# Kernel tuning notes

Measured on AMD Instinct MI355X. Metric: run time of the kernel, lower is better.

Reference implementation:

```python
import jax, jax.numpy as jnp
import numpy as np

B, D = 16, 8192
CH = 32
N_BLOCKS = 24
DILATIONS = [2 ** i for i in range(8)] * 3  # 3 stacks of 8 layers


def _causal_conv(x, W, b, dilation):
    # x: (B, Cin, L); W: (Cout, Cin, K). Causal = left-pad (K-1)*dilation only,
    # which equals torch's symmetric-pad-then-slice-right trick.
    pad = (W.shape[-1] - 1) * dilation
    y = jax.lax.conv_general_dilated(
        x, W, window_strides=(1,), padding=[(pad, 0)],
        rhs_dilation=(dilation,), dimension_numbers=('NCH', 'OIH', 'NCH'))
    return y + b[None, :, None]


def setup_inputs() -> dict:
    key = jax.random.key(0)
    ks = jax.random.split(key, 13)
    s = 0.1  # keep activations in a sane range
    return {
        'x': jax.random.normal(ks[0], (B, D), jnp.float32),
        'W0': jax.random.normal(ks[1], (CH, 1, 2), jnp.float32) * s,
        'b0': jax.random.normal(ks[2], (CH,), jnp.float32) * s,
        'Wd': jax.random.normal(ks[3], (N_BLOCKS, 2 * CH, CH, 2), jnp.float32) * s,
        'bd': jax.random.normal(ks[4], (N_BLOCKS, 2 * CH), jnp.float32) * s,
        'W1': jax.random.normal(ks[5], (N_BLOCKS, CH, CH), jnp.float32) * s,
        'b1': jax.random.normal(ks[6], (N_BLOCKS, CH), jnp.float32) * s,
        'Wf': jax.random.normal(ks[7], (CH, CH), jnp.float32) * s,
        'bf': jax.random.normal(ks[8], (CH,), jnp.float32) * s,
        'fW1': jax.random.normal(ks[9], (64, CH * 4), jnp.float32) * s,
        'fb1': jax.random.normal(ks[10], (64,), jnp.float32) * s,
        'fW2': jax.random.normal(ks[11], (10, 64), jnp.float32) * s,
        'fb2': jax.random.normal(ks[12], (10,), jnp.float32) * s,
    }


def reference(x, W0, b0, Wd, bd, W1, b1, Wf, bf, fW1, fb1, fW2, fb2):
    h = _causal_conv(x[:, None, :], W0, b0, 1)  # (B, 32, L)
    skip_sum = jnp.zeros_like(h)
    for i, dil in enumerate(DILATIONS):
        z = _causal_conv(h, Wd[i], bd[i], dil)          # (B, 64, L)
        f, g = jnp.split(z, 2, axis=1)
        gated = jnp.tanh(f) * jax.nn.sigmoid(g)          # (B, 32, L)
        skip = jnp.einsum('oc,bcl->bol', W1[i], gated) + b1[i][None, :, None]
        h = h + skip                                     # residual (dropout = eval identity)
        skip_sum = skip_sum + skip                       # sum of stacked skips
    y = jax.nn.relu(skip_sum)
    y = jnp.einsum('oc,bcl->bol', Wf, y) + bf[None, :, None]
    y = jax.nn.relu(y)
    # AdaptiveMaxPool1d(4): L divisible by 4 -> max over contiguous chunks
    Bc, C, L = y.shape
    y = y.reshape(Bc, C, 4, L // 4).max(axis=-1)         # (B, 32, 4)
    y = y.reshape(Bc, C * 4)
    y = jax.nn.relu(y @ fW1.T + fb1)
    return y @ fW2.T + fb2
```

## Files before the change

kernel.cpp:

```cpp
#include <hip/hip_runtime.h>
#include <hip/hip_bf16.h>

#define BATCH 16
#define SEQ 8192
#define CH 32
#define NB 24

typedef __attribute__((ext_vector_type(8))) short short8;
typedef __attribute__((ext_vector_type(4))) short short4v;
typedef __attribute__((ext_vector_type(4))) float f32x4;

#define LROW 36

__device__ __forceinline__ unsigned short f2bf(float x) {
    __hip_bfloat16 b = __float2bfloat16(x);
    unsigned short u;
    __builtin_memcpy(&u, &b, 2);
    return u;
}
__device__ __forceinline__ float bf2f(unsigned short h) {
    return __uint_as_float(((unsigned int)h) << 16);
}
__device__ __forceinline__ float rcp_fast(float x) { return __builtin_amdgcn_rcpf(x); }

__device__ __forceinline__ float gate_fn(float f, float g) {
    float ef = __expf(-2.0f * fabsf(f));
    float eg = __expf(-g);
    float num = 1.0f - ef;
    float den = (1.0f + ef) * (1.0f + eg);
    return copysignf(num * rcp_fast(den), f);
}

__device__ __forceinline__ void split2(float v, unsigned short& h, unsigned short& l) {
    h = f2bf(v);
    l = f2bf(v - bf2f(h));
}

__global__ __launch_bounds__(64) void k_prep(const float* __restrict__ Wd,
                                             const float* __restrict__ bd,
                                             const float* __restrict__ W1,
                                             const float* __restrict__ b1,
                                             unsigned short* __restrict__ stream) {
    int i = blockIdx.x;
    int l = threadIdx.x;
    int p = l & 15, h4 = l >> 4;
    const float* wd  = Wd + (size_t)i * 64 * 64;
    const float* w1  = W1 + (size_t)i * 1024;
    const float* bdp = bd + (size_t)i * 64;
    const float* b1p = b1 + (size_t)i * 32;
    unsigned short* out = stream + (size_t)i * (28672 / 2);

    for (int rt = 0; rt < 4; ++rt)
        for (int q = 0; q < 2; ++q) {
            int slot = rt * 2 + q;
            for (int j = 0; j < 8; ++j) {
                int m = 16 * rt + p;
                int k = 32 * q + 8 * h4 + j;
                int c = k & 31, tap = k >> 5;
                float w = wd[m * 64 + c * 2 + tap];
                unsigned short hi = f2bf(w);
                out[(size_t)slot * 512 + l * 8 + j] = hi;
                out[(size_t)(8 + slot) * 512 + l * 8 + j] = f2bf(w - bf2f(hi));
            }
        }
    for (int rt2 = 0; rt2 < 2; ++rt2)
        for (int j = 0; j < 8; ++j) {
            int o = 16 * rt2 + p, c = 8 * h4 + j;
            float w = w1[o * 32 + c];
            unsigned short hi = f2bf(w);
            out[(size_t)(16 + rt2) * 512 + l * 8 + j] = hi;
            out[(size_t)(18 + rt2) * 512 + l * 8 + j] = f2bf(w - bf2f(hi));
        }
    float* outf = (float*)stream + (size_t)i * (28672 / 4);
    for (int rt = 0; rt < 4; ++rt)
        for (int r = 0; r < 4; ++r)
            outf[(size_t)(20 + rt) * 256 + l * 4 + r] = bdp[16 * rt + 4 * h4 + r];
    for (int rt2 = 0; rt2 < 2; ++rt2)
        for (int r = 0; r < 4; ++r)
            outf[(size_t)(24 + rt2) * 256 + l * 4 + r] = b1p[16 * rt2 + 4 * h4 + r];
}

__global__ __launch_bounds__(256) void k_init(const float* __restrict__ x,
                                              const float* __restrict__ W0,
                                              const float* __restrict__ b0,
                                              float* __restrict__ h,
                                              float* __restrict__ pooled) {
    int idx = blockIdx.x * 256 + threadIdx.x;
    int b = idx >> 13, t = idx & (SEQ - 1);
    float xt = x[b * SEQ + t];
    float xm = (t > 0) ? x[b * SEQ + t - 1] : 0.0f;
    __align__(16) float hv[CH];
#pragma unroll
    for (int c = 0; c < CH; ++c)
        hv[c] = W0[c * 2] * xm + W0[c * 2 + 1] * xt + b0[c];
    float* dst = h + (size_t)idx * CH;
#pragma unroll
    for (int k = 0; k < 8; ++k)
        *(f32x4*)(dst + 4 * k) = *(const f32x4*)(hv + 4 * k);
    if (idx < BATCH * CH * 4) pooled[idx] = 0.0f;
}

__global__ __launch_bounds__(512, 2) void k_stack(
        const float* __restrict__ hin,
        float* __restrict__ hout,
        const unsigned short* __restrict__ wstream,
        int stack) {
    __shared__ __align__(16) float lh[768 * LROW];
    __shared__ __align__(16) unsigned short gbuf[8][2][16][40];

    int tid = threadIdx.x;
    int lane = tid & 63, wave = tid >> 6;
    int p = lane & 15, h4 = lane >> 4;
    int bb = blockIdx.x >> 4;
    int T0 = (blockIdx.x & 15) * 512;

    const float* pin = hin + (size_t)bb * SEQ * CH;
    float* pout = hout + (size_t)bb * SEQ * CH;

    const f32x4 zero4 = {0.0f, 0.0f, 0.0f, 0.0f};

    for (int i = tid; i < 768; i += 512) {
        int t = T0 - 256 + i;
        float* dst = &lh[i * LROW];
        if (t >= 0) {
            const float* src = pin + (size_t)t * CH;
#pragma unroll
            for (int k = 0; k < 8; ++k)
                *(f32x4*)(dst + 4 * k) = *(const f32x4*)(src + 4 * k);
        } else {
#pragma unroll
            for (int k = 0; k < 8; ++k)
                *(f32x4*)(dst + 4 * k) = zero4;
        }
    }
    __syncthreads();

#pragma unroll 1
    for (int l = 0; l < 8; ++l) {
        int dil = 1 << l;
        const unsigned short* frag = wstream + (size_t)(8 * stack + l) * 14336;
        const short8* fs = (const short8*)frag;
        short8 Ah[4][2], Al[4][2], Sh[2], Sl[2];
#pragma unroll
        for (int rt = 0; rt < 4; ++rt)
#pragma unroll
            for (int q = 0; q < 2; ++q) {
                Ah[rt][q] = fs[(rt * 2 + q) * 64 + lane];
                Al[rt][q] = fs[(8 + rt * 2 + q) * 64 + lane];
            }
#pragma unroll
        for (int rt2 = 0; rt2 < 2; ++rt2) {
            Sh[rt2] = fs[(16 + rt2) * 64 + lane];
            Sl[rt2] = fs[(18 + rt2) * 64 + lane];
        }
        const f32x4* ff = (const f32x4*)frag;
        f32x4 bFG[4], bS[2];
#pragma unroll
        for (int rt = 0; rt < 4; ++rt) bFG[rt] = ff[(20 + rt) * 64 + lane];
#pragma unroll
        for (int rt2 = 0; rt2 < 2; ++rt2) bS[rt2] = ff[(24 + rt2) * 64 + lane];

        f32x4 hnew[6][2];

#pragma unroll
        for (int s6 = 0; s6 < 6; ++s6) {
            int tpos = wave * 96 + s6 * 16 + p;
            int tq = tpos - dil;
            bool ok = (T0 - 256 + tq >= 0);
            int tqc = (tq > 0) ? tq : 0;

            const float* r1 = &lh[tpos * LROW + 8 * h4];
            const float* r0 = &lh[tqc * LROW + 8 * h4];
            f32x4 v1a = *(const f32x4*)r1, v1b = *(const f32x4*)(r1 + 4);
            f32x4 v0a = *(const f32x4*)r0, v0b = *(const f32x4*)(r0 + 4);
            if (!ok) { v0a = zero4; v0b = zero4; }
            short8 bh1, bl1, bh0, bl0;
#pragma unroll
            for (int j = 0; j < 4; ++j) {
                unsigned short hh, ll;
                split2(v1a[j], hh, ll); bh1[j] = (short)hh; bl1[j] = (short)ll;
                split2(v1b[j], hh, ll); bh1[4 + j] = (short)hh; bl1[4 + j] = (short)ll;
                split2(v0a[j], hh, ll); bh0[j] = (short)hh; bl0[j] = (short)ll;
                split2(v0b[j], hh, ll); bh0[4 + j] = (short)hh; bl0[4 + j] = (short)ll;
            }

            f32x4 acc[4];
#pragma unroll
            for (int rt = 0; rt < 4; ++rt) {
                f32x4 a = bFG[rt];
                a = __builtin_amdgcn_mfma_f32_16x16x32_bf16(Ah[rt][0], bh0, a, 0, 0, 0);
                a = __builtin_amdgcn_mfma_f32_16x16x32_bf16(Ah[rt][1], bh1, a, 0, 0, 0);
                a = __builtin_amdgcn_mfma_f32_16x16x32_bf16(Ah[rt][0], bl0, a, 0, 0, 0);
                a = __builtin_amdgcn_mfma_f32_16x16x32_bf16(Ah[rt][1], bl1, a, 0, 0, 0);
                a = __builtin_amdgcn_mfma_f32_16x16x32_bf16(Al[rt][0], bh0, a, 0, 0, 0);
                a = __builtin_amdgcn_mfma_f32_16x16x32_bf16(Al[rt][1], bh1, a, 0, 0, 0);
                acc[rt] = a;
            }

#pragma unroll
            for (int rt = 0; rt < 2; ++rt) {
                __align__(8) unsigned short g4h[4], g4l[4];
#pragma unroll
                for (int r = 0; r < 4; ++r) {
                    float gated = gate_fn(acc[rt][r], acc[rt + 2][r]);
                    split2(gated, g4h[r], g4l[r]);
                }
                *(short4v*)&gbuf[wave][0][p][16 * rt + 4 * h4] = *(const short4v*)g4h;
                *(short4v*)&gbuf[wave][1][p][16 * rt + 4 * h4] = *(const short4v*)g4l;
            }
            asm volatile("s_waitcnt lgkmcnt(0)" ::: "memory");
            __builtin_amdgcn_sched_barrier(0);
            short8 Bgh = *(const short8*)&gbuf[wave][0][p][8 * h4];
            short8 Bgl = *(const short8*)&gbuf[wave][1][p][8 * h4];

            f32x4 sacc[2];
#pragma unroll
            for (int rt2 = 0; rt2 < 2; ++rt2) {
                f32x4 a = bS[rt2];
                a = __builtin_amdgcn_mfma_f32_16x16x32_bf16(Sh[rt2], Bgh, a, 0, 0, 0);
                a = __builtin_amdgcn_mfma_f32_16x16x32_bf16(Sh[rt2], Bgl, a, 0, 0, 0);
                a = __builtin_amdgcn_mfma_f32_16x16x32_bf16(Sl[rt2], Bgh, a, 0, 0, 0);
                sacc[rt2] = a;
            }

#pragma unroll
            for (int rt2 = 0; rt2 < 2; ++rt2) {
                f32x4 hold = *(const f32x4*)&lh[tpos * LROW + 16 * rt2 + 4 * h4];
                hnew[s6][rt2] = hold + sacc[rt2];
            }
        }
        __syncthreads();

#pragma unroll
        for (int s6 = 0; s6 < 6; ++s6) {
            int tpos = wave * 96 + s6 * 16 + p;
#pragma unroll
            for (int rt2 = 0; rt2 < 2; ++rt2)
                *(f32x4*)&lh[tpos * LROW + 16 * rt2 + 4 * h4] = hnew[s6][rt2];
        }
        __syncthreads();
    }

    {
        int i = 256 + tid;
        int t = T0 + tid;
        const float* src = &lh[i * LROW];
        float* dst = pout + (size_t)t * CH;
#pragma unroll
        for (int k = 0; k < 8; ++k)
            *(f32x4*)(dst + 4 * k) = *(const f32x4*)(src + 4 * k);
    }
}

__global__ __launch_bounds__(256) void k_final1(
        const float* __restrict__ hfin,
        const float* __restrict__ x,
        const float* __restrict__ W0,
        const float* __restrict__ b0,
        const float* __restrict__ Wf,
        const float* __restrict__ bf,
        float* __restrict__ pooled) {
    int blk = blockIdx.x;
    int b = blk >> 5;
    int chunk = blk & 31;
    int q = chunk >> 3;
    int t = chunk * 256 + threadIdx.x;

    float xt = x[b * SEQ + t];
    float xm = (t > 0) ? x[b * SEQ + t - 1] : 0.0f;
    const float* ph = hfin + ((size_t)b * SEQ + t) * CH;
    f32x4 v[8];
#pragma unroll
    for (int k = 0; k < 8; ++k) v[k] = *(const f32x4*)(ph + 4 * k);

    float r[CH];
#pragma unroll
    for (int k = 0; k < 8; ++k)
#pragma unroll
        for (int j = 0; j < 4; ++j) {
            int c = 4 * k + j;
            float h0 = W0[c * 2] * xm + W0[c * 2 + 1] * xt + b0[c];
            r[c] = fmaxf(v[k][j] - h0, 0.0f);
        }

    float y[CH];
#pragma unroll 1
    for (int o = 0; o < CH; ++o) {
        const float* w = Wf + o * CH;
        float a0 = bf[o], a1 = 0.0f, a2 = 0.0f, a3 = 0.0f;
#pragma unroll
        for (int c = 0; c < CH; c += 4) {
            a0 += w[c + 0] * r[c + 0];
            a1 += w[c + 1] * r[c + 1];
            a2 += w[c + 2] * r[c + 2];
            a3 += w[c + 3] * r[c + 3];
        }
        y[o] = fmaxf((a0 + a1) + (a2 + a3), 0.0f);
    }

#pragma unroll
    for (int o = 0; o < CH; ++o) {
#pragma unroll
        for (int off = 32; off >= 1; off >>= 1)
            y[o] = fmaxf(y[o], __shfl_xor(y[o], off));
    }

    __shared__ float red[4 * CH];
    int wave = threadIdx.x >> 6, lane = threadIdx.x & 63;
    if (lane == 0) {
#pragma unroll
        for (int o = 0; o < CH; ++o) red[wave * CH + o] = y[o];
    }
    __syncthreads();
    if (threadIdx.x < CH) {
        float m = fmaxf(fmaxf(red[threadIdx.x], red[CH + threadIdx.x]),
                        fmaxf(red[2 * CH + threadIdx.x], red[3 * CH + threadIdx.x]));
        atomicMax((unsigned int*)&pooled[b * (CH * 4) + threadIdx.x * 4 + q],
                  __float_as_uint(m));
    }
}

__global__ __launch_bounds__(1024) void k_final2(const float* __restrict__ pooled,
                                                 const float* __restrict__ fW1,
                                                 const float* __restrict__ fb1,
                                                 const float* __restrict__ fW2,
                                                 const float* __restrict__ fb2,
                                                 float* __restrict__ out) {
    __shared__ float y1[BATCH * 64];
    int tid = threadIdx.x;
    int b = tid >> 6, o = tid & 63;
    float acc = fb1[o];
#pragma unroll
    for (int j = 0; j < 128; ++j) acc += fW1[o * 128 + j] * pooled[b * 128 + j];
    y1[b * 64 + o] = fmaxf(acc, 0.0f);
    __syncthreads();
    if (tid < BATCH * 10) {
        int bb = tid / 10, o2 = tid % 10;
        float a2 = fb2[o2];
#pragma unroll
        for (int j = 0; j < 64; ++j) a2 += fW2[o2 * 64 + j] * y1[bb * 64 + j];
        out[bb * 10 + o2] = a2;
    }
}

extern "C" void kernel_launch(void* const* d_in, const int* in_sizes, int n_in,
                              void* d_out, int out_size, void* d_ws, size_t ws_size,
                              hipStream_t stream) {
    const float* x   = (const float*)d_in[0];
    const float* W0  = (const float*)d_in[1];
    const float* b0  = (const float*)d_in[2];
    const float* Wd  = (const float*)d_in[3];
    const float* bd  = (const float*)d_in[4];
    const float* W1  = (const float*)d_in[5];
    const float* b1  = (const float*)d_in[6];
    const float* Wf  = (const float*)d_in[7];
    const float* bf  = (const float*)d_in[8];
    const float* fW1 = (const float*)d_in[9];
    const float* fb1 = (const float*)d_in[10];
    const float* fW2 = (const float*)d_in[11];
    const float* fb2 = (const float*)d_in[12];
    float* out = (float*)d_out;

    const size_t HS = (size_t)BATCH * SEQ * CH;
    float* bufA = (float*)d_ws;
    float* bufB = bufA + HS;
    unsigned short* wstream = (unsigned short*)(bufB + HS);
    float* pooled = (float*)(wstream + (size_t)NB * 14336);

    k_prep<<<NB, 64, 0, stream>>>(Wd, bd, W1, b1, wstream);
    k_init<<<512, 256, 0, stream>>>(x, W0, b0, bufA, pooled);

    k_stack<<<256, 512, 0, stream>>>(bufA, bufB, wstream, 0);
    k_stack<<<256, 512, 0, stream>>>(bufB, bufA, wstream, 1);
    k_stack<<<256, 512, 0, stream>>>(bufA, bufB, wstream, 2);

    k_final1<<<512, 256, 0, stream>>>(bufB, x, W0, b0, Wf, bf, pooled);
    k_final2<<<1, 1024, 0, stream>>>(pooled, fW1, fb1, fW2, fb2, out);
}
```

Before: 365.7 us.

## Fuse init and final pooling into stack kernels, software-pipeline skip MFMA

Removes k_init by computing the first conv inside the first k_stack launch from x, and removes k_final1 by doing the final 1x1 conv, ReLU and max-pool reduction inside the last stack launch, skipping its hidden-state write-back. Pooled zeroing moves into k_prep. The per-layer inner loop is software-pipelined: the gbuf is double-buffered so the skip MFMA for slice i-1 overlaps the dilated-conv MFMA for slice i. This saves two launches and a full HBM round trip of the hidden state, at the cost of more shared memory and register pressure in k_stack.

```diff
diff --git a/kernel.cpp b/kernel.cpp
--- a/kernel.cpp
+++ b/kernel.cpp
@@ -40,7 +40,8 @@
                                              const float* __restrict__ bd,
                                              const float* __restrict__ W1,
                                              const float* __restrict__ b1,
-                                             unsigned short* __restrict__ stream) {
+                                             unsigned short* __restrict__ stream,
+                                             float* __restrict__ pooled) {
     int i = blockIdx.x;
     int l = threadIdx.x;
     int p = l & 15, h4 = l >> 4;
@@ -49,6 +50,9 @@
     const float* bdp = bd + (size_t)i * 64;
     const float* b1p = b1 + (size_t)i * 32;
     unsigned short* out = stream + (size_t)i * (28672 / 2);
+
+    for (int g = blockIdx.x * 64 + l; g < BATCH * CH * 4; g += NB * 64)
+        pooled[g] = 0.0f;
 
     for (int rt = 0; rt < 4; ++rt)
         for (int q = 0; q < 2; ++q) {
@@ -80,57 +84,69 @@
             outf[(size_t)(24 + rt2) * 256 + l * 4 + r] = b1p[16 * rt2 + 4 * h4 + r];
 }
 
-__global__ __launch_bounds__(256) void k_init(const float* __restrict__ x,
-                                              const float* __restrict__ W0,
-                                              const float* __restrict__ b0,
-                                              float* __restrict__ h,
-                                              float* __restrict__ pooled) {
-    int idx = blockIdx.x * 256 + threadIdx.x;
-    int b = idx >> 13, t = idx & (SEQ - 1);
-    float xt = x[b * SEQ + t];
-    float xm = (t > 0) ? x[b * SEQ + t - 1] : 0.0f;
-    __align__(16) float hv[CH];
-#pragma unroll
-    for (int c = 0; c < CH; ++c)
-        hv[c] = W0[c * 2] * xm + W0[c * 2 + 1] * xt + b0[c];
-    float* dst = h + (size_t)idx * CH;
-#pragma unroll
-    for (int k = 0; k < 8; ++k)
-        *(f32x4*)(dst + 4 * k) = *(const f32x4*)(hv + 4 * k);
-    if (idx < BATCH * CH * 4) pooled[idx] = 0.0f;
-}
-
 __global__ __launch_bounds__(512, 2) void k_stack(
         const float* __restrict__ hin,
         float* __restrict__ hout,
+        const float* __restrict__ x,
+        const float* __restrict__ W0,
+        const float* __restrict__ b0,
+        const float* __restrict__ Wf,
+        const float* __restrict__ bf,
+        float* __restrict__ pooled,
         const unsigned short* __restrict__ wstream,
         int stack) {
     __shared__ __align__(16) float lh[768 * LROW];
-    __shared__ __align__(16) unsigned short gbuf[8][2][16][40];
+    __shared__ __align__(16) unsigned short gbuf[8][2][2][16][40];
+    __shared__ float red[8 * CH];
 
     int tid = threadIdx.x;
     int lane = tid & 63, wave = tid >> 6;
     int p = lane & 15, h4 = lane >> 4;
     int bb = blockIdx.x >> 4;
     int T0 = (blockIdx.x & 15) * 512;
+    bool first = (stack == 0);
+    bool last  = (stack == 2);
 
     const float* pin = hin + (size_t)bb * SEQ * CH;
     float* pout = hout + (size_t)bb * SEQ * CH;
+    const float* px = x + (size_t)bb * SEQ;
 
     const f32x4 zero4 = {0.0f, 0.0f, 0.0f, 0.0f};
 
-    for (int i = tid; i < 768; i += 512) {
-        int t = T0 - 256 + i;
-        float* dst = &lh[i * LROW];
-        if (t >= 0) {
-            const float* src = pin + (size_t)t * CH;
-#pragma unroll
-            for (int k = 0; k < 8; ++k)
-                *(f32x4*)(dst + 4 * k) = *(const f32x4*)(src + 4 * k);
-        } else {
-#pragma unroll
-            for (int k = 0; k < 8; ++k)
-                *(f32x4*)(dst + 4 * k) = zero4;
+    if (first) {
+        for (int i = tid; i < 768; i += 512) {
+            int t = T0 - 256 + i;
+            float* dst = &lh[i * LROW];
+            if (t >= 0) {
+                float xt = px[t];
+                float xm = (t > 0) ? px[t - 1] : 0.0f;
+                __align__(16) float hv[CH];
+#pragma unroll
+                for (int c = 0; c < CH; ++c)
+                    hv[c] = W0[c * 2] * xm + W0[c * 2 + 1] * xt + b0[c];
+#pragma unroll
+                for (int k = 0; k < 8; ++k)
+                    *(f32x4*)(dst + 4 * k) = *(const f32x4*)(hv + 4 * k);
+            } else {
+#pragma unroll
+                for (int k = 0; k < 8; ++k)
+                    *(f32x4*)(dst + 4 * k) = zero4;
+            }
+        }
+    } else {
+        for (int i = tid; i < 768; i += 512) {
+            int t = T0 - 256 + i;
+            float* dst = &lh[i * LROW];
+            if (t >= 0) {
+                const float* src = pin + (size_t)t * CH;
+#pragma unroll
+                for (int k = 0; k < 8; ++k)
+                    *(f32x4*)(dst + 4 * k) = *(const f32x4*)(src + 4 * k);
+            } else {
+#pragma unroll
+                for (int k = 0; k < 8; ++k)
+                    *(f32x4*)(dst + 4 * k) = zero4;
+            }
         }
     }
     __syncthreads();
@@ -163,77 +179,83 @@
         f32x4 hnew[6][2];
 
 #pragma unroll
+        for (int i = 0; i < 7; ++i) {
+            f32x4 acc[4];
+            if (i < 6) {
+                int tpos = wave * 96 + i * 16 + p;
+                int tq = tpos - dil;
+                bool ok = (T0 - 256 + tq >= 0);
+                int tqc = (tq > 0) ? tq : 0;
+
+                const float* r1 = &lh[tpos * LROW + 8 * h4];
+                const float* r0 = &lh[tqc * LROW + 8 * h4];
+                f32x4 v1a = *(const f32x4*)r1, v1b = *(const f32x4*)(r1 + 4);
+                f32x4 v0a = *(const f32x4*)r0, v0b = *(const f32x4*)(r0 + 4);
+                if (!ok) { v0a = zero4; v0b = zero4; }
+                short8 bh1, bl1, bh0, bl0;
+#pragma unroll
+                for (int j = 0; j < 4; ++j) {
+                    unsigned short hh, ll;
+                    split2(v1a[j], hh, ll); bh1[j] = (short)hh; bl1[j] = (short)ll;
+                    split2(v1b[j], hh, ll); bh1[4 + j] = (short)hh; bl1[4 + j] = (short)ll;
+                    split2(v0a[j], hh, ll); bh0[j] = (short)hh; bl0[j] = (short)ll;
+                    split2(v0b[j], hh, ll); bh0[4 + j] = (short)hh; bl0[4 + j] = (short)ll;
+                }
+#pragma unroll
+                for (int rt = 0; rt < 4; ++rt) {
+                    f32x4 a = bFG[rt];
+                    a = __builtin_amdgcn_mfma_f32_16x16x32_bf16(Ah[rt][0], bh0, a, 0, 0, 0);
+                    a = __builtin_amdgcn_mfma_f32_16x16x32_bf16(Ah[rt][1], bh1, a, 0, 0, 0);
+                    a = __builtin_amdgcn_mfma_f32_16x16x32_bf16(Ah[rt][0], bl0, a, 0, 0, 0);
+                    a = __builtin_amdgcn_mfma_f32_16x16x32_bf16(Ah[rt][1], bl1, a, 0, 0, 0);
+                    a = __builtin_amdgcn_mfma_f32_16x16x32_bf16(Al[rt][0], bh0, a, 0, 0, 0);
+                    a = __builtin_amdgcn_mfma_f32_16x16x32_bf16(Al[rt][1], bh1, a, 0, 0, 0);
+                    acc[rt] = a;
+                }
+            }
+
+            if (i > 0) {
+                asm volatile("s_waitcnt lgkmcnt(0)" ::: "memory");
+                int ip = i - 1;
+                int tposP = wave * 96 + ip * 16 + p;
+                short8 Bgh = *(const short8*)&gbuf[wave][ip & 1][0][p][8 * h4];
+                short8 Bgl = *(const short8*)&gbuf[wave][ip & 1][1][p][8 * h4];
+
+                f32x4 sacc[2];
+#pragma unroll
+                for (int rt2 = 0; rt2 < 2; ++rt2) {
+                    f32x4 a = bS[rt2];
+                    a = __builtin_amdgcn_mfma_f32_16x16x32_bf16(Sh[rt2], Bgh, a, 0, 0, 0);
+                    a = __builtin_amdgcn_mfma_f32_16x16x32_bf16(Sh[rt2], Bgl, a, 0, 0, 0);
+                    a = __builtin_amdgcn_mfma_f32_16x16x32_bf16(Sl[rt2], Bgh, a, 0, 0, 0);
+                    sacc[rt2] = a;
+                }
+#pragma unroll
+                for (int rt2 = 0; rt2 < 2; ++rt2) {
+                    f32x4 hold = *(const f32x4*)&lh[tposP * LROW + 16 * rt2 + 4 * h4];
+                    hnew[ip][rt2] = hold + sacc[rt2];
+                }
+            }
+
+            if (i < 6) {
+#pragma unroll
+                for (int rt = 0; rt < 2; ++rt) {
+                    __align__(8) unsigned short g4h[4], g4l[4];
+#pragma unroll
+                    for (int r = 0; r < 4; ++r) {
+                        float gated = gate_fn(acc[rt][r], acc[rt + 2][r]);
+                        split2(gated, g4h[r], g4l[r]);
+                    }
+                    *(short4v*)&gbuf[wave][i & 1][0][p][16 * rt + 4 * h4] = *(const short4v*)g4h;
+                    *(short4v*)&gbuf[wave][i & 1][1][p][16 * rt + 4 * h4] = *(const short4v*)g4l;
+                }
+            }
+        }
+        __syncthreads();
+
+#pragma unroll
         for (int s6 = 0; s6 < 6; ++s6) {
             int tpos = wave * 96 + s6 * 16 + p;
-            int tq = tpos - dil;
-            bool ok = (T0 - 256 + tq >= 0);
-            int tqc = (tq > 0) ? tq : 0;
-
-            const float* r1 = &lh[tpos * LROW + 8 * h4];
-            const float* r0 = &lh[tqc * LROW + 8 * h4];
-            f32x4 v1a = *(const f32x4*)r1, v1b = *(const f32x4*)(r1 + 4);
-            f32x4 v0a = *(const f32x4*)r0, v0b = *(const f32x4*)(r0 + 4);
-            if (!ok) { v0a = zero4; v0b = zero4; }
-            short8 bh1, bl1, bh0, bl0;
-#pragma unroll
-            for (int j = 0; j < 4; ++j) {
-                unsigned short hh, ll;
-                split2(v1a[j], hh, ll); bh1[j] = (short)hh; bl1[j] = (short)ll;
-                split2(v1b[j], hh, ll); bh1[4 + j] = (short)hh; bl1[4 + j] = (short)ll;
-                split2(v0a[j], hh, ll); bh0[j] = (short)hh; bl0[j] = (short)ll;
-                split2(v0b[j], hh, ll); bh0[4 + j] = (short)hh; bl0[4 + j] = (short)ll;
-            }
-
-            f32x4 acc[4];
-#pragma unroll
-            for (int rt = 0; rt < 4; ++rt) {
-                f32x4 a = bFG[rt];
-                a = __builtin_amdgcn_mfma_f32_16x16x32_bf16(Ah[rt][0], bh0, a, 0, 0, 0);
-                a = __builtin_amdgcn_mfma_f32_16x16x32_bf16(Ah[rt][1], bh1, a, 0, 0, 0);
-                a = __builtin_amdgcn_mfma_f32_16x16x32_bf16(Ah[rt][0], bl0, a, 0, 0, 0);
-                a = __builtin_amdgcn_mfma_f32_16x16x32_bf16(Ah[rt][1], bl1, a, 0, 0, 0);
-                a = __builtin_amdgcn_mfma_f32_16x16x32_bf16(Al[rt][0], bh0, a, 0, 0, 0);
-                a = __builtin_amdgcn_mfma_f32_16x16x32_bf16(Al[rt][1], bh1, a, 0, 0, 0);
-                acc[rt] = a;
-            }
-
-#pragma unroll
-            for (int rt = 0; rt < 2; ++rt) {
-                __align__(8) unsigned short g4h[4], g4l[4];
-#pragma unroll
-                for (int r = 0; r < 4; ++r) {
-                    float gated = gate_fn(acc[rt][r], acc[rt + 2][r]);
-                    split2(gated, g4h[r], g4l[r]);
-                }
-                *(short4v*)&gbuf[wave][0][p][16 * rt + 4 * h4] = *(const short4v*)g4h;
-                *(short4v*)&gbuf[wave][1][p][16 * rt + 4 * h4] = *(const short4v*)g4l;
-            }
-            asm volatile("s_waitcnt lgkmcnt(0)" ::: "memory");
-            __builtin_amdgcn_sched_barrier(0);
-            short8 Bgh = *(const short8*)&gbuf[wave][0][p][8 * h4];
-            short8 Bgl = *(const short8*)&gbuf[wave][1][p][8 * h4];
-
-            f32x4 sacc[2];
-#pragma unroll
-            for (int rt2 = 0; rt2 < 2; ++rt2) {
-                f32x4 a = bS[rt2];
-                a = __builtin_amdgcn_mfma_f32_16x16x32_bf16(Sh[rt2], Bgh, a, 0, 0, 0);
-                a = __builtin_amdgcn_mfma_f32_16x16x32_bf16(Sh[rt2], Bgl, a, 0, 0, 0);
-                a = __builtin_amdgcn_mfma_f32_16x16x32_bf16(Sl[rt2], Bgh, a, 0, 0, 0);
-                sacc[rt2] = a;
-            }
-
-#pragma unroll
-            for (int rt2 = 0; rt2 < 2; ++rt2) {
-                f32x4 hold = *(const f32x4*)&lh[tpos * LROW + 16 * rt2 + 4 * h4];
-                hnew[s6][rt2] = hold + sacc[rt2];
-            }
-        }
-        __syncthreads();
-
-#pragma unroll
-        for (int s6 = 0; s6 < 6; ++s6) {
-            int tpos = wave * 96 + s6 * 16 + p;
 #pragma unroll
             for (int rt2 = 0; rt2 < 2; ++rt2)
                 *(f32x4*)&lh[tpos * LROW + 16 * rt2 + 4 * h4] = hnew[s6][rt2];
@@ -241,7 +263,7 @@
         __syncthreads();
     }
 
-    {
+    if (!last) {
         int i = 256 + tid;
         int t = T0 + tid;
         const float* src = &lh[i * LROW];
@@ -249,74 +271,52 @@
 #pragma unroll
         for (int k = 0; k < 8; ++k)
             *(f32x4*)(dst + 4 * k) = *(const f32x4*)(src + 4 * k);
-    }
-}
-
-__global__ __launch_bounds__(256) void k_final1(
-        const float* __restrict__ hfin,
-        const float* __restrict__ x,
-        const float* __restrict__ W0,
-        const float* __restrict__ b0,
-        const float* __restrict__ Wf,
-        const float* __restrict__ bf,
-        float* __restrict__ pooled) {
-    int blk = blockIdx.x;
-    int b = blk >> 5;
-    int chunk = blk & 31;
-    int q = chunk >> 3;
-    int t = chunk * 256 + threadIdx.x;
-
-    float xt = x[b * SEQ + t];
-    float xm = (t > 0) ? x[b * SEQ + t - 1] : 0.0f;
-    const float* ph = hfin + ((size_t)b * SEQ + t) * CH;
-    f32x4 v[8];
-#pragma unroll
-    for (int k = 0; k < 8; ++k) v[k] = *(const f32x4*)(ph + 4 * k);
-
-    float r[CH];
-#pragma unroll
-    for (int k = 0; k < 8; ++k)
-#pragma unroll
-        for (int j = 0; j < 4; ++j) {
-            int c = 4 * k + j;
+    } else {
+        int i = 256 + tid;
+        int t = T0 + tid;
+        int q = (blockIdx.x & 15) >> 2;
+        float xt = px[t];
+        float xm = (t > 0) ? px[t - 1] : 0.0f;
+        const float* src = &lh[i * LROW];
+
+        float r[CH];
+#pragma unroll
+        for (int c = 0; c < CH; ++c) {
             float h0 = W0[c * 2] * xm + W0[c * 2 + 1] * xt + b0[c];
-            r[c] = fmaxf(v[k][j] - h0, 0.0f);
-        }
-
-    float y[CH];
+            r[c] = fmaxf(src[c] - h0, 0.0f);
+        }
+        float y[CH];
 #pragma unroll 1
-    for (int o = 0; o < CH; ++o) {
-        const float* w = Wf + o * CH;
-        float a0 = bf[o], a1 = 0.0f, a2 = 0.0f, a3 = 0.0f;
-#pragma unroll
-        for (int c = 0; c < CH; c += 4) {
-            a0 += w[c + 0] * r[c + 0];
-            a1 += w[c + 1] * r[c + 1];
-            a2 += w[c + 2] * r[c + 2];
-            a3 += w[c + 3] * r[c + 3];
-        }
-        y[o] = fmaxf((a0 + a1) + (a2 + a3), 0.0f);
-    }
-
-#pragma unroll
-    for (int o = 0; o < CH; ++o) {
-#pragma unroll
-        for (int off = 32; off >= 1; off >>= 1)
-            y[o] = fmaxf(y[o], __shfl_xor(y[o], off));
-    }
-
-    __shared__ float red[4 * CH];
-    int wave = threadIdx.x >> 6, lane = threadIdx.x & 63;
-    if (lane == 0) {
-#pragma unroll
-        for (int o = 0; o < CH; ++o) red[wave * CH + o] = y[o];
-    }
-    __syncthreads();
-    if (threadIdx.x < CH) {
-        float m = fmaxf(fmaxf(red[threadIdx.x], red[CH + threadIdx.x]),
-                        fmaxf(red[2 * CH + threadIdx.x], red[3 * CH + threadIdx.x]));
-        atomicMax((unsigned int*)&pooled[b * (CH * 4) + threadIdx.x * 4 + q],
-                  __float_as_uint(m));
+        for (int o = 0; o < CH; ++o) {
+            const float* w = Wf + o * CH;
+            float a0 = bf[o], a1 = 0.0f, a2 = 0.0f, a3 = 0.0f;
+#pragma unroll
+            for (int c = 0; c < CH; c += 4) {
+                a0 += w[c + 0] * r[c + 0];
+                a1 += w[c + 1] * r[c + 1];
+                a2 += w[c + 2] * r[c + 2];
+                a3 += w[c + 3] * r[c + 3];
+            }
+            y[o] = fmaxf((a0 + a1) + (a2 + a3), 0.0f);
+        }
+#pragma unroll
+        for (int o = 0; o < CH; ++o) {
+#pragma unroll
+            for (int off = 32; off >= 1; off >>= 1)
+                y[o] = fmaxf(y[o], __shfl_xor(y[o], off));
+        }
+        if (lane == 0) {
+#pragma unroll
+            for (int o = 0; o < CH; ++o) red[wave * CH + o] = y[o];
+        }
+        __syncthreads();
+        if (tid < CH) {
+            float m = red[tid];
+#pragma unroll
+            for (int w8 = 1; w8 < 8; ++w8) m = fmaxf(m, red[w8 * CH + tid]);
+            atomicMax((unsigned int*)&pooled[bb * (CH * 4) + tid * 4 + q],
+                      __float_as_uint(m));
+        }
     }
 }
 
@@ -367,13 +367,11 @@
     unsigned short* wstream = (unsigned short*)(bufB + HS);
     float* pooled = (float*)(wstream + (size_t)NB * 14336);
 
-    k_prep<<<NB, 64, 0, stream>>>(Wd, bd, W1, b1, wstream);
-    k_init<<<512, 256, 0, stream>>>(x, W0, b0, bufA, pooled);
-
-    k_stack<<<256, 512, 0, stream>>>(bufA, bufB, wstream, 0);
-    k_stack<<<256, 512, 0, stream>>>(bufB, bufA, wstream, 1);
-    k_stack<<<256, 512, 0, stream>>>(bufA, bufB, wstream, 2);
-
-    k_final1<<<512, 256, 0, stream>>>(bufB, x, W0, b0, Wf, bf, pooled);
+    k_prep<<<NB, 64, 0, stream>>>(Wd, bd, W1, b1, wstream, pooled);
+
+    k_stack<<<256, 512, 0, stream>>>(bufA, bufB, x, W0, b0, Wf, bf, pooled, wstream, 0);
+    k_stack<<<256, 512, 0, stream>>>(bufB, bufA, x, W0, b0, Wf, bf, pooled, wstream, 1);
+    k_stack<<<256, 512, 0, stream>>>(bufA, bufA, x, W0, b0, Wf, bf, pooled, wstream, 2);
+
     k_final2<<<1, 1024, 0, stream>>>(pooled, fW1, fb1, fW2, fb2, out);
 }
```

Result: faster. 328.3 us (-10.2%).
